# Kernel tuning notes

Measured on AMD Instinct MI355X. Metric: run time of the kernel, lower is better.

Reference implementation:

```python
import jax, jax.numpy as jnp
import numpy as np

N_NODES = 100000
N_EDGES = 1600000
NUM_FEATS = 128
HIDDEN = 16
NUM_CLASSES = 40


def setup_inputs() -> dict:
    key = jax.random.key(0)
    k1, k2, k3, k4, k5 = jax.random.split(key, 5)
    x = jax.random.normal(k1, (N_NODES, NUM_FEATS), dtype=jnp.float32)
    edge_weight = jax.random.uniform(k2, (N_EDGES,), dtype=jnp.float32)
    # Glorot-uniform linear weights (bias=False in the module)
    lim1 = float(np.sqrt(6.0 / (NUM_FEATS + HIDDEN)))
    lim2 = float(np.sqrt(6.0 / (HIDDEN + NUM_CLASSES)))
    W1 = jax.random.uniform(k3, (NUM_FEATS, HIDDEN), dtype=jnp.float32, minval=-lim1, maxval=lim1)
    W2 = jax.random.uniform(k4, (HIDDEN, NUM_CLASSES), dtype=jnp.float32, minval=-lim2, maxval=lim2)
    edge_index = jax.random.randint(k5, (2, N_EDGES), 0, N_NODES, dtype=jnp.int64)
    return {"x": x, "edge_weight": edge_weight, "W1": W1, "W2": W2, "edge_index": edge_index}


def _sgconv(h, W, src, dst, edge_weight, n):
    # SGConv (K=1): weighted neighbor aggregation + self loop (weight 1), then bias-free linear
    msg = edge_weight[:, None] * h[src]                      # [E, d] gather + scale
    agg = jax.ops.segment_sum(msg, dst, num_segments=n) + h  # scatter-add + self loop
    return agg @ W


def reference(x, edge_weight, W1, W2, edge_index):
    src, dst = edge_index[0], edge_index[1]
    n = x.shape[0]
    h = _sgconv(x, W1, src, dst, edge_weight, n)   # [N, 16]
    # dropout(p=0.5) is identity in eval mode
    h = _sgconv(h, W2, src, dst, edge_weight, n)   # [N, num_classes]
    return jax.nn.log_softmax(h, axis=1)
```

## Files before the change

kernel.cpp:

```cpp
#include <hip/hip_runtime.h>

#define NFEAT 128
#define HID 16
#define NCLS 40
#define BSHIFT 7
#define BNODES 128
#define CAP 2560
#define NBUCK_MAX 800
#define BIN_CHUNK 4096

#define SCALE1 262144.0f
#define SCALE2 65536.0f

__device__ __forceinline__ unsigned bf16_rne(float f) {
    unsigned u = __float_as_uint(f);
    return (u + 0x7FFFu + ((u >> 16) & 1u)) >> 16;
}
__device__ __forceinline__ float bf_lo(unsigned u) { return __uint_as_float(u << 16); }
__device__ __forceinline__ float bf_hi(unsigned u) { return __uint_as_float(u & 0xFFFF0000u); }


__global__ __launch_bounds__(256) void init_cursor_kernel(int* __restrict__ cursor, int nbuck)
{
    int i = blockIdx.x * 256 + threadIdx.x;
    if (i < nbuck) cursor[i] = i * CAP;
}

__global__ __launch_bounds__(256) void bin_kernel(const int* __restrict__ src,
                                                  const int* __restrict__ dst,
                                                  const float* __restrict__ ew,
                                                  int* __restrict__ cursor,
                                                  int2* __restrict__ slab,
                                                  int E, int nbuck)
{
    __shared__ int hist[NBUCK_MAX];
    __shared__ int runbase[NBUCK_MAX];
    int tid = threadIdx.x;
    for (int i = tid; i < NBUCK_MAX; i += 256) hist[i] = 0;
    __syncthreads();

    int base = blockIdx.x * BIN_CHUNK;
    int myd[16], mys[16], myw[16];
    #pragma unroll
    for (int k = 0; k < 16; ++k) {
        int e = base + k * 256 + tid;
        if (e < E) {
            myd[k] = dst[e];
            mys[k] = src[e];
            myw[k] = __float_as_int(ew[e]);
            atomicAdd(&hist[myd[k] >> BSHIFT], 1);
        } else myd[k] = -1;
    }
    __syncthreads();
    for (int i = tid; i < nbuck; i += 256) {
        int c = hist[i];
        runbase[i] = c ? atomicAdd(&cursor[i], c) : 0;
        hist[i] = 0;
    }
    __syncthreads();
    #pragma unroll
    for (int k = 0; k < 16; ++k) {
        int d = myd[k];
        if (d >= 0) {
            int b = d >> BSHIFT;
            int pos = runbase[b] + atomicAdd(&hist[b], 1);
            if (pos < (b + 1) * CAP)
                slab[pos] = make_int2(mys[k] | ((d & (BNODES - 1)) << 20), myw[k]);
        }
    }
}


__global__ __launch_bounds__(256) void gemm1_kernel(const float* __restrict__ x,
                                                    const float* __restrict__ W1,
                                                    unsigned short* __restrict__ h1b, int n)
{
    __shared__ float xs[64 * 132];
    __shared__ float ws[16 * 132];
    int tid = threadIdx.x;
    int r0 = blockIdx.x * 64;
    int rows = n - r0; if (rows > 64) rows = 64;

    const float4* xg = (const float4*)(x + (size_t)r0 * NFEAT);
    #pragma unroll
    for (int i = 0; i < 8; ++i) {
        int flat4 = i * 256 + tid;
        int row = flat4 >> 5, k4 = flat4 & 31;
        float4 v = make_float4(0.f, 0.f, 0.f, 0.f);
        if (row < rows) v = xg[flat4];
        *(float4*)&xs[row * 132 + k4 * 4] = v;
    }
    for (int i = tid; i < HID * NFEAT; i += 256) {
        int c = i >> 7, k = i & 127;
        ws[c * 132 + k] = W1[k * HID + c];
    }
    __syncthreads();

    int row = tid >> 2;
    int c0  = (tid & 3) * 4;
    float acc[4] = {0.f, 0.f, 0.f, 0.f};
    #pragma unroll 4
    for (int k4 = 0; k4 < 32; ++k4) {
        float4 xv = *(const float4*)&xs[row * 132 + k4 * 4];
        #pragma unroll
        for (int i = 0; i < 4; ++i) {
            float4 wv = *(const float4*)&ws[(c0 + i) * 132 + k4 * 4];
            acc[i] += xv.x * wv.x + xv.y * wv.y + xv.z * wv.z + xv.w * wv.w;
        }
    }
    if (row < rows) {
        unsigned lo = bf16_rne(acc[0]) | (bf16_rne(acc[1]) << 16);
        unsigned hi = bf16_rne(acc[2]) | (bf16_rne(acc[3]) << 16);
        *(uint2*)(h1b + (size_t)(r0 + row) * HID + c0) = make_uint2(lo, hi);
    }
}

__global__ __launch_bounds__(512) void gather_int_kernel(const uint4* __restrict__ hq,
                                                         const int* __restrict__ cursor,
                                                         const int2* __restrict__ slab,
                                                         float scale,
                                                         float4* __restrict__ outf,
                                                         uint4* __restrict__ outb,
                                                         int n)
{
    __shared__ int accum[HID * BNODES];
    int tid = threadIdx.x;
    #pragma unroll
    for (int i = tid; i < HID * BNODES; i += 512) accum[i] = 0;
    __syncthreads();

    int b = blockIdx.x;
    int beg = b * CAP;
    int cnt = cursor[b] - beg;
    if (cnt > CAP) cnt = CAP;

    int tasks = cnt * 2;
    for (int i = tid; i < tasks; i += 512) {
        int2 e = slab[beg + (i >> 1)];
        int p = i & 1;
        int s  = e.x & 0xFFFFF;
        int dl = (e.x >> 20) & (BNODES - 1);
        float wsc = __int_as_float(e.y) * scale;
        uint4 q = hq[(size_t)s * 2 + p];
        int* a = &accum[(p * 8) * BNODES + dl];
        atomicAdd(a + 0 * BNODES, __float2int_rn(wsc * bf_lo(q.x)));
        atomicAdd(a + 1 * BNODES, __float2int_rn(wsc * bf_hi(q.x)));
        atomicAdd(a + 2 * BNODES, __float2int_rn(wsc * bf_lo(q.y)));
        atomicAdd(a + 3 * BNODES, __float2int_rn(wsc * bf_hi(q.y)));
        atomicAdd(a + 4 * BNODES, __float2int_rn(wsc * bf_lo(q.z)));
        atomicAdd(a + 5 * BNODES, __float2int_rn(wsc * bf_hi(q.z)));
        atomicAdd(a + 6 * BNODES, __float2int_rn(wsc * bf_lo(q.w)));
        atomicAdd(a + 7 * BNODES, __float2int_rn(wsc * bf_hi(q.w)));
    }
    __syncthreads();

    float inv = 1.0f / scale;
    if (tid < BNODES * 2) {
        int dl = tid >> 1, p = tid & 1;
        int node = (b << BSHIFT) + dl;
        if (node < n) {
            uint4 qs = hq[(size_t)node * 2 + p];
            const int* a = &accum[(p * 8) * BNODES + dl];
            float r[8];
            r[0] = (float)a[0 * BNODES] * inv + bf_lo(qs.x);
            r[1] = (float)a[1 * BNODES] * inv + bf_hi(qs.x);
            r[2] = (float)a[2 * BNODES] * inv + bf_lo(qs.y);
            r[3] = (float)a[3 * BNODES] * inv + bf_hi(qs.y);
            r[4] = (float)a[4 * BNODES] * inv + bf_lo(qs.z);
            r[5] = (float)a[5 * BNODES] * inv + bf_hi(qs.z);
            r[6] = (float)a[6 * BNODES] * inv + bf_lo(qs.w);
            r[7] = (float)a[7 * BNODES] * inv + bf_hi(qs.w);
            if (outf) {
                outf[(size_t)node * 4 + p * 2 + 0] = make_float4(r[0], r[1], r[2], r[3]);
                outf[(size_t)node * 4 + p * 2 + 1] = make_float4(r[4], r[5], r[6], r[7]);
            }
            if (outb) {
                uint4 o;
                o.x = bf16_rne(r[0]) | (bf16_rne(r[1]) << 16);
                o.y = bf16_rne(r[2]) | (bf16_rne(r[3]) << 16);
                o.z = bf16_rne(r[4]) | (bf16_rne(r[5]) << 16);
                o.w = bf16_rne(r[6]) | (bf16_rne(r[7]) << 16);
                outb[(size_t)node * 2 + p] = o;
            }
        }
    }
}

__global__ __launch_bounds__(256) void gemm2_lsm_kernel(const float* __restrict__ h,
                                                        const float* __restrict__ W2,
                                                        float* __restrict__ out, int n)
{
    __shared__ float ws[HID * NCLS];
    int tid = threadIdx.x;
    for (int i = tid; i < HID * NCLS; i += 256) ws[i] = W2[i];
    __syncthreads();
    int r = blockIdx.x * 256 + tid;
    if (r >= n) return;

    float hr[HID];
    const float4* h4 = (const float4*)(h + (size_t)r * HID);
    #pragma unroll
    for (int i = 0; i < 4; ++i) {
        float4 v = h4[i];
        hr[i * 4 + 0] = v.x; hr[i * 4 + 1] = v.y; hr[i * 4 + 2] = v.z; hr[i * 4 + 3] = v.w;
    }
    float acc[NCLS];
    #pragma unroll
    for (int j = 0; j < NCLS; ++j) acc[j] = 0.f;
    #pragma unroll
    for (int k = 0; k < HID; ++k) {
        float hk = hr[k];
        #pragma unroll
        for (int j4 = 0; j4 < NCLS / 4; ++j4) {
            float4 w = *(const float4*)&ws[k * NCLS + j4 * 4];
            acc[j4 * 4 + 0] += hk * w.x;
            acc[j4 * 4 + 1] += hk * w.y;
            acc[j4 * 4 + 2] += hk * w.z;
            acc[j4 * 4 + 3] += hk * w.w;
        }
    }
    float m = acc[0];
    #pragma unroll
    for (int j = 1; j < NCLS; ++j) m = fmaxf(m, acc[j]);
    float ssum = 0.f;
    #pragma unroll
    for (int j = 0; j < NCLS; ++j) ssum += __expf(acc[j] - m);
    float l = m + __logf(ssum);
    float4* o4 = (float4*)(out + (size_t)r * NCLS);
    #pragma unroll
    for (int j4 = 0; j4 < NCLS / 4; ++j4)
        o4[j4] = make_float4(acc[j4 * 4 + 0] - l, acc[j4 * 4 + 1] - l,
                             acc[j4 * 4 + 2] - l, acc[j4 * 4 + 3] - l);
}

extern "C" void kernel_launch(void* const* d_in, const int* in_sizes, int n_in,
                              void* d_out, int out_size, void* d_ws, size_t ws_size,
                              hipStream_t stream)
{
    const float* x  = (const float*)d_in[0];
    const float* ew = (const float*)d_in[1];
    const float* W1 = (const float*)d_in[2];
    const float* W2 = (const float*)d_in[3];
    const int*   ei = (const int*)d_in[4];

    int n = in_sizes[0] / NFEAT;
    int E = in_sizes[1];
    const int* src = ei;
    const int* dst = ei + E;
    float* out = (float*)d_out;

    int nbuck = (n + BNODES - 1) >> BSHIFT;
    int nbin  = (E + BIN_CHUNK - 1) / BIN_CHUNK;

    char* w = (char*)d_ws;
    int*  cursor = (int*)w;  w += NBUCK_MAX * 4;
    w = (char*)(((size_t)w + 15) & ~(size_t)15);
    int2* slab   = (int2*)w; w += (size_t)NBUCK_MAX * CAP * 8;
    unsigned short* h1b = (unsigned short*)w; w += (size_t)n * HID * 2;
    unsigned short* h2b = (unsigned short*)w; w += (size_t)n * HID * 2;
    float* g2           = (float*)w;          w += (size_t)n * HID * 4;

    init_cursor_kernel<<<(nbuck + 255) / 256, 256, 0, stream>>>(cursor, nbuck);
    bin_kernel<<<nbin, 256, 0, stream>>>(src, dst, ew, cursor, slab, E, nbuck);

    gemm1_kernel<<<(n + 63) / 64, 256, 0, stream>>>(x, W1, h1b, n);
    gather_int_kernel<<<nbuck, 512, 0, stream>>>((const uint4*)h1b, cursor, slab,
                                                 SCALE1, nullptr, (uint4*)h2b, n);
    gather_int_kernel<<<nbuck, 512, 0, stream>>>((const uint4*)h2b, cursor, slab,
                                                 SCALE2, (float4*)g2, nullptr, n);
    gemm2_lsm_kernel<<<(n + 255) / 256, 256, 0, stream>>>(g2, W2, out, n);
}
```

Before: 185.2 us.

## Fuse binning with GEMM1 and second gather with GEMM2 plus log-softmax

Merges the edge-binning kernel and the first dense projection into one launch, where blocks are split by block index so both run concurrently. The second gather is fused with the W2 projection and log-softmax, so the fp32 intermediate no longer makes a round trip through global memory. The init-cursor kernel becomes a memset, with cursors now holding relative counts. This cuts launch count and intermediate traffic, at the cost of higher shared-memory and register use in the fused gather, where only 128 of 512 threads do the per-node epilogue.

```diff
diff --git a/kernel.cpp b/kernel.cpp
--- a/kernel.cpp
+++ b/kernel.cpp
@@ -20,108 +20,96 @@
 __device__ __forceinline__ float bf_hi(unsigned u) { return __uint_as_float(u & 0xFFFF0000u); }
 
 
-__global__ __launch_bounds__(256) void init_cursor_kernel(int* __restrict__ cursor, int nbuck)
-{
-    int i = blockIdx.x * 256 + threadIdx.x;
-    if (i < nbuck) cursor[i] = i * CAP;
-}
-
-__global__ __launch_bounds__(256) void bin_kernel(const int* __restrict__ src,
-                                                  const int* __restrict__ dst,
-                                                  const float* __restrict__ ew,
-                                                  int* __restrict__ cursor,
-                                                  int2* __restrict__ slab,
-                                                  int E, int nbuck)
-{
-    __shared__ int hist[NBUCK_MAX];
-    __shared__ int runbase[NBUCK_MAX];
+__global__ __launch_bounds__(256) void fused_bin_gemm1_kernel(
+        const int* __restrict__ src, const int* __restrict__ dst,
+        const float* __restrict__ ew, int* __restrict__ cursor,
+        int2* __restrict__ slab, int E, int nbuck, int nbin,
+        const float* __restrict__ x, const float* __restrict__ W1,
+        unsigned short* __restrict__ h1b, int n)
+{
+    __shared__ float smem[80 * 132];
     int tid = threadIdx.x;
-    for (int i = tid; i < NBUCK_MAX; i += 256) hist[i] = 0;
-    __syncthreads();
-
-    int base = blockIdx.x * BIN_CHUNK;
-    int myd[16], mys[16], myw[16];
-    #pragma unroll
-    for (int k = 0; k < 16; ++k) {
-        int e = base + k * 256 + tid;
-        if (e < E) {
-            myd[k] = dst[e];
-            mys[k] = src[e];
-            myw[k] = __float_as_int(ew[e]);
-            atomicAdd(&hist[myd[k] >> BSHIFT], 1);
-        } else myd[k] = -1;
-    }
-    __syncthreads();
-    for (int i = tid; i < nbuck; i += 256) {
-        int c = hist[i];
-        runbase[i] = c ? atomicAdd(&cursor[i], c) : 0;
-        hist[i] = 0;
-    }
-    __syncthreads();
-    #pragma unroll
-    for (int k = 0; k < 16; ++k) {
-        int d = myd[k];
-        if (d >= 0) {
-            int b = d >> BSHIFT;
-            int pos = runbase[b] + atomicAdd(&hist[b], 1);
-            if (pos < (b + 1) * CAP)
-                slab[pos] = make_int2(mys[k] | ((d & (BNODES - 1)) << 20), myw[k]);
-        }
-    }
-}
-
-
-__global__ __launch_bounds__(256) void gemm1_kernel(const float* __restrict__ x,
-                                                    const float* __restrict__ W1,
-                                                    unsigned short* __restrict__ h1b, int n)
-{
-    __shared__ float xs[64 * 132];
-    __shared__ float ws[16 * 132];
-    int tid = threadIdx.x;
-    int r0 = blockIdx.x * 64;
-    int rows = n - r0; if (rows > 64) rows = 64;
-
-    const float4* xg = (const float4*)(x + (size_t)r0 * NFEAT);
-    #pragma unroll
-    for (int i = 0; i < 8; ++i) {
-        int flat4 = i * 256 + tid;
-        int row = flat4 >> 5, k4 = flat4 & 31;
-        float4 v = make_float4(0.f, 0.f, 0.f, 0.f);
-        if (row < rows) v = xg[flat4];
-        *(float4*)&xs[row * 132 + k4 * 4] = v;
-    }
-    for (int i = tid; i < HID * NFEAT; i += 256) {
-        int c = i >> 7, k = i & 127;
-        ws[c * 132 + k] = W1[k * HID + c];
-    }
-    __syncthreads();
-
-    int row = tid >> 2;
-    int c0  = (tid & 3) * 4;
-    float acc[4] = {0.f, 0.f, 0.f, 0.f};
-    #pragma unroll 4
-    for (int k4 = 0; k4 < 32; ++k4) {
-        float4 xv = *(const float4*)&xs[row * 132 + k4 * 4];
+
+    if (blockIdx.x < (unsigned)nbin) {
+        int* hist    = (int*)smem;
+        int* runbase = hist + NBUCK_MAX;
+        for (int i = tid; i < NBUCK_MAX; i += 256) hist[i] = 0;
+        __syncthreads();
+
+        int base = blockIdx.x * BIN_CHUNK;
+        int myd[16], mys[16], myw[16];
         #pragma unroll
-        for (int i = 0; i < 4; ++i) {
-            float4 wv = *(const float4*)&ws[(c0 + i) * 132 + k4 * 4];
-            acc[i] += xv.x * wv.x + xv.y * wv.y + xv.z * wv.z + xv.w * wv.w;
-        }
-    }
-    if (row < rows) {
-        unsigned lo = bf16_rne(acc[0]) | (bf16_rne(acc[1]) << 16);
-        unsigned hi = bf16_rne(acc[2]) | (bf16_rne(acc[3]) << 16);
-        *(uint2*)(h1b + (size_t)(r0 + row) * HID + c0) = make_uint2(lo, hi);
-    }
-}
-
-__global__ __launch_bounds__(512) void gather_int_kernel(const uint4* __restrict__ hq,
-                                                         const int* __restrict__ cursor,
-                                                         const int2* __restrict__ slab,
-                                                         float scale,
-                                                         float4* __restrict__ outf,
-                                                         uint4* __restrict__ outb,
-                                                         int n)
+        for (int k = 0; k < 16; ++k) {
+            int e = base + k * 256 + tid;
+            if (e < E) {
+                myd[k] = dst[e];
+                mys[k] = src[e];
+                myw[k] = __float_as_int(ew[e]);
+                atomicAdd(&hist[myd[k] >> BSHIFT], 1);
+            } else myd[k] = -1;
+        }
+        __syncthreads();
+        for (int i = tid; i < nbuck; i += 256) {
+            int c = hist[i];
+            runbase[i] = c ? (i * CAP + atomicAdd(&cursor[i], c)) : 0;
+            hist[i] = 0;
+        }
+        __syncthreads();
+        #pragma unroll
+        for (int k = 0; k < 16; ++k) {
+            int d = myd[k];
+            if (d >= 0) {
+                int b = d >> BSHIFT;
+                int pos = runbase[b] + atomicAdd(&hist[b], 1);
+                if (pos < (b + 1) * CAP)
+                    slab[pos] = make_int2(mys[k] | ((d & (BNODES - 1)) << 20), myw[k]);
+            }
+        }
+    } else {
+        float* xs = smem;
+        float* ws = smem + 64 * 132;
+        int r0 = (blockIdx.x - nbin) * 64;
+        int rows = n - r0; if (rows > 64) rows = 64;
+
+        const float4* xg = (const float4*)(x + (size_t)r0 * NFEAT);
+        #pragma unroll
+        for (int i = 0; i < 8; ++i) {
+            int flat4 = i * 256 + tid;
+            int row = flat4 >> 5, k4 = flat4 & 31;
+            float4 v = make_float4(0.f, 0.f, 0.f, 0.f);
+            if (row < rows) v = xg[flat4];
+            *(float4*)&xs[row * 132 + k4 * 4] = v;
+        }
+        for (int i = tid; i < HID * NFEAT; i += 256) {
+            int c = i >> 7, k = i & 127;
+            ws[c * 132 + k] = W1[k * HID + c];
+        }
+        __syncthreads();
+
+        int row = tid >> 2;
+        int c0  = (tid & 3) * 4;
+        float acc[4] = {0.f, 0.f, 0.f, 0.f};
+        #pragma unroll 4
+        for (int k4 = 0; k4 < 32; ++k4) {
+            float4 xv = *(const float4*)&xs[row * 132 + k4 * 4];
+            #pragma unroll
+            for (int i = 0; i < 4; ++i) {
+                float4 wv = *(const float4*)&ws[(c0 + i) * 132 + k4 * 4];
+                acc[i] += xv.x * wv.x + xv.y * wv.y + xv.z * wv.z + xv.w * wv.w;
+            }
+        }
+        if (row < rows) {
+            unsigned lo = bf16_rne(acc[0]) | (bf16_rne(acc[1]) << 16);
+            unsigned hi = bf16_rne(acc[2]) | (bf16_rne(acc[3]) << 16);
+            *(uint2*)(h1b + (size_t)(r0 + row) * HID + c0) = make_uint2(lo, hi);
+        }
+    }
+}
+
+__global__ __launch_bounds__(512) void gather1_kernel(const uint4* __restrict__ hq,
+                                                      const int* __restrict__ cursor,
+                                                      const int2* __restrict__ slab,
+                                                      uint4* __restrict__ outb, int n)
 {
     __shared__ int accum[HID * BNODES];
     int tid = threadIdx.x;
@@ -131,8 +119,7 @@
 
     int b = blockIdx.x;
     int beg = b * CAP;
-    int cnt = cursor[b] - beg;
-    if (cnt > CAP) cnt = CAP;
+    int cnt = cursor[b]; if (cnt > CAP) cnt = CAP;
 
     int tasks = cnt * 2;
     for (int i = tid; i < tasks; i += 512) {
@@ -140,7 +127,7 @@
         int p = i & 1;
         int s  = e.x & 0xFFFFF;
         int dl = (e.x >> 20) & (BNODES - 1);
-        float wsc = __int_as_float(e.y) * scale;
+        float wsc = __int_as_float(e.y) * SCALE1;
         uint4 q = hq[(size_t)s * 2 + p];
         int* a = &accum[(p * 8) * BNODES + dl];
         atomicAdd(a + 0 * BNODES, __float2int_rn(wsc * bf_lo(q.x)));
@@ -154,83 +141,121 @@
     }
     __syncthreads();
 
-    float inv = 1.0f / scale;
+    const float inv = 1.0f / SCALE1;
     if (tid < BNODES * 2) {
         int dl = tid >> 1, p = tid & 1;
         int node = (b << BSHIFT) + dl;
         if (node < n) {
             uint4 qs = hq[(size_t)node * 2 + p];
             const int* a = &accum[(p * 8) * BNODES + dl];
-            float r[8];
-            r[0] = (float)a[0 * BNODES] * inv + bf_lo(qs.x);
-            r[1] = (float)a[1 * BNODES] * inv + bf_hi(qs.x);
-            r[2] = (float)a[2 * BNODES] * inv + bf_lo(qs.y);
-            r[3] = (float)a[3 * BNODES] * inv + bf_hi(qs.y);
-            r[4] = (float)a[4 * BNODES] * inv + bf_lo(qs.z);
-            r[5] = (float)a[5 * BNODES] * inv + bf_hi(qs.z);
-            r[6] = (float)a[6 * BNODES] * inv + bf_lo(qs.w);
-            r[7] = (float)a[7 * BNODES] * inv + bf_hi(qs.w);
-            if (outf) {
-                outf[(size_t)node * 4 + p * 2 + 0] = make_float4(r[0], r[1], r[2], r[3]);
-                outf[(size_t)node * 4 + p * 2 + 1] = make_float4(r[4], r[5], r[6], r[7]);
+            uint4 o;
+            o.x = bf16_rne((float)a[0 * BNODES] * inv + bf_lo(qs.x)) |
+                  (bf16_rne((float)a[1 * BNODES] * inv + bf_hi(qs.x)) << 16);
+            o.y = bf16_rne((float)a[2 * BNODES] * inv + bf_lo(qs.y)) |
+                  (bf16_rne((float)a[3 * BNODES] * inv + bf_hi(qs.y)) << 16);
+            o.z = bf16_rne((float)a[4 * BNODES] * inv + bf_lo(qs.z)) |
+                  (bf16_rne((float)a[5 * BNODES] * inv + bf_hi(qs.z)) << 16);
+            o.w = bf16_rne((float)a[6 * BNODES] * inv + bf_lo(qs.w)) |
+                  (bf16_rne((float)a[7 * BNODES] * inv + bf_hi(qs.w)) << 16);
+            outb[(size_t)node * 2 + p] = o;
+        }
+    }
+}
+
+#define ZPAD 41
+__global__ __launch_bounds__(512) void gather2_lsm_kernel(const uint4* __restrict__ hq,
+                                                          const int* __restrict__ cursor,
+                                                          const int2* __restrict__ slab,
+                                                          const float* __restrict__ W2,
+                                                          float* __restrict__ out, int n)
+{
+    __shared__ int   accum[HID * BNODES];
+    __shared__ float w2s[HID * NCLS];
+    __shared__ float zbuf[BNODES * ZPAD];
+    int tid = threadIdx.x;
+    #pragma unroll
+    for (int i = tid; i < HID * BNODES; i += 512) accum[i] = 0;
+    for (int i = tid; i < HID * NCLS; i += 512) w2s[i] = W2[i];
+    __syncthreads();
+
+    int b = blockIdx.x;
+    int beg = b * CAP;
+    int cnt = cursor[b]; if (cnt > CAP) cnt = CAP;
+    int node0 = b << BSHIFT;
+
+    int tasks = cnt * 2;
+    for (int i = tid; i < tasks; i += 512) {
+        int2 e = slab[beg + (i >> 1)];
+        int p = i & 1;
+        int s  = e.x & 0xFFFFF;
+        int dl = (e.x >> 20) & (BNODES - 1);
+        float wsc = __int_as_float(e.y) * SCALE2;
+        uint4 q = hq[(size_t)s * 2 + p];
+        int* a = &accum[(p * 8) * BNODES + dl];
+        atomicAdd(a + 0 * BNODES, __float2int_rn(wsc * bf_lo(q.x)));
+        atomicAdd(a + 1 * BNODES, __float2int_rn(wsc * bf_hi(q.x)));
+        atomicAdd(a + 2 * BNODES, __float2int_rn(wsc * bf_lo(q.y)));
+        atomicAdd(a + 3 * BNODES, __float2int_rn(wsc * bf_hi(q.y)));
+        atomicAdd(a + 4 * BNODES, __float2int_rn(wsc * bf_lo(q.z)));
+        atomicAdd(a + 5 * BNODES, __float2int_rn(wsc * bf_hi(q.z)));
+        atomicAdd(a + 6 * BNODES, __float2int_rn(wsc * bf_lo(q.w)));
+        atomicAdd(a + 7 * BNODES, __float2int_rn(wsc * bf_hi(q.w)));
+    }
+    __syncthreads();
+
+    const float inv = 1.0f / SCALE2;
+    if (tid < BNODES) {
+        int dl = tid;
+        int node = node0 + dl;
+        if (node < n) {
+            uint4 q0 = hq[(size_t)node * 2 + 0];
+            uint4 q1 = hq[(size_t)node * 2 + 1];
+            float r[HID];
+            r[0]  = (float)accum[ 0 * BNODES + dl] * inv + bf_lo(q0.x);
+            r[1]  = (float)accum[ 1 * BNODES + dl] * inv + bf_hi(q0.x);
+            r[2]  = (float)accum[ 2 * BNODES + dl] * inv + bf_lo(q0.y);
+            r[3]  = (float)accum[ 3 * BNODES + dl] * inv + bf_hi(q0.y);
+            r[4]  = (float)accum[ 4 * BNODES + dl] * inv + bf_lo(q0.z);
+            r[5]  = (float)accum[ 5 * BNODES + dl] * inv + bf_hi(q0.z);
+            r[6]  = (float)accum[ 6 * BNODES + dl] * inv + bf_lo(q0.w);
+            r[7]  = (float)accum[ 7 * BNODES + dl] * inv + bf_hi(q0.w);
+            r[8]  = (float)accum[ 8 * BNODES + dl] * inv + bf_lo(q1.x);
+            r[9]  = (float)accum[ 9 * BNODES + dl] * inv + bf_hi(q1.x);
+            r[10] = (float)accum[10 * BNODES + dl] * inv + bf_lo(q1.y);
+            r[11] = (float)accum[11 * BNODES + dl] * inv + bf_hi(q1.y);
+            r[12] = (float)accum[12 * BNODES + dl] * inv + bf_lo(q1.z);
+            r[13] = (float)accum[13 * BNODES + dl] * inv + bf_hi(q1.z);
+            r[14] = (float)accum[14 * BNODES + dl] * inv + bf_lo(q1.w);
+            r[15] = (float)accum[15 * BNODES + dl] * inv + bf_hi(q1.w);
+
+            float z[NCLS];
+            #pragma unroll
+            for (int j = 0; j < NCLS; ++j) z[j] = 0.f;
+            #pragma unroll
+            for (int f = 0; f < HID; ++f) {
+                float rf = r[f];
+                #pragma unroll
+                for (int j = 0; j < NCLS; ++j)
+                    z[j] += rf * w2s[f * NCLS + j];
             }
-            if (outb) {
-                uint4 o;
-                o.x = bf16_rne(r[0]) | (bf16_rne(r[1]) << 16);
-                o.y = bf16_rne(r[2]) | (bf16_rne(r[3]) << 16);
-                o.z = bf16_rne(r[4]) | (bf16_rne(r[5]) << 16);
-                o.w = bf16_rne(r[6]) | (bf16_rne(r[7]) << 16);
-                outb[(size_t)node * 2 + p] = o;
-            }
-        }
-    }
-}
-
-__global__ __launch_bounds__(256) void gemm2_lsm_kernel(const float* __restrict__ h,
-                                                        const float* __restrict__ W2,
-                                                        float* __restrict__ out, int n)
-{
-    __shared__ float ws[HID * NCLS];
-    int tid = threadIdx.x;
-    for (int i = tid; i < HID * NCLS; i += 256) ws[i] = W2[i];
-    __syncthreads();
-    int r = blockIdx.x * 256 + tid;
-    if (r >= n) return;
-
-    float hr[HID];
-    const float4* h4 = (const float4*)(h + (size_t)r * HID);
-    #pragma unroll
-    for (int i = 0; i < 4; ++i) {
-        float4 v = h4[i];
-        hr[i * 4 + 0] = v.x; hr[i * 4 + 1] = v.y; hr[i * 4 + 2] = v.z; hr[i * 4 + 3] = v.w;
-    }
-    float acc[NCLS];
-    #pragma unroll
-    for (int j = 0; j < NCLS; ++j) acc[j] = 0.f;
-    #pragma unroll
-    for (int k = 0; k < HID; ++k) {
-        float hk = hr[k];
-        #pragma unroll
-        for (int j4 = 0; j4 < NCLS / 4; ++j4) {
-            float4 w = *(const float4*)&ws[k * NCLS + j4 * 4];
-            acc[j4 * 4 + 0] += hk * w.x;
-            acc[j4 * 4 + 1] += hk * w.y;
-            acc[j4 * 4 + 2] += hk * w.z;
-            acc[j4 * 4 + 3] += hk * w.w;
-        }
-    }
-    float m = acc[0];
-    #pragma unroll
-    for (int j = 1; j < NCLS; ++j) m = fmaxf(m, acc[j]);
-    float ssum = 0.f;
-    #pragma unroll
-    for (int j = 0; j < NCLS; ++j) ssum += __expf(acc[j] - m);
-    float l = m + __logf(ssum);
-    float4* o4 = (float4*)(out + (size_t)r * NCLS);
-    #pragma unroll
-    for (int j4 = 0; j4 < NCLS / 4; ++j4)
-        o4[j4] = make_float4(acc[j4 * 4 + 0] - l, acc[j4 * 4 + 1] - l,
-                             acc[j4 * 4 + 2] - l, acc[j4 * 4 + 3] - l);
+            float m = z[0];
+            #pragma unroll
+            for (int j = 1; j < NCLS; ++j) m = fmaxf(m, z[j]);
+            float ssum = 0.f;
+            #pragma unroll
+            for (int j = 0; j < NCLS; ++j) ssum += __expf(z[j] - m);
+            float l = m + __logf(ssum);
+            #pragma unroll
+            for (int j = 0; j < NCLS; ++j) zbuf[dl * ZPAD + j] = z[j] - l;
+        }
+    }
+    __syncthreads();
+
+    for (int i = tid; i < BNODES * NCLS; i += 512) {
+        int nl = i / NCLS, j = i - nl * NCLS;
+        if (node0 + nl < n)
+            out[(size_t)node0 * NCLS + i] = zbuf[nl * ZPAD + j];
+    }
 }
 
 extern "C" void kernel_launch(void* const* d_in, const int* in_sizes, int n_in,
@@ -251,6 +276,7 @@
 
     int nbuck = (n + BNODES - 1) >> BSHIFT;
     int nbin  = (E + BIN_CHUNK - 1) / BIN_CHUNK;
+    int ngemm = (n + 63) / 64;
 
     char* w = (char*)d_ws;
     int*  cursor = (int*)w;  w += NBUCK_MAX * 4;
@@ -258,15 +284,12 @@
     int2* slab   = (int2*)w; w += (size_t)NBUCK_MAX * CAP * 8;
     unsigned short* h1b = (unsigned short*)w; w += (size_t)n * HID * 2;
     unsigned short* h2b = (unsigned short*)w; w += (size_t)n * HID * 2;
-    float* g2           = (float*)w;          w += (size_t)n * HID * 4;
-
-    init_cursor_kernel<<<(nbuck + 255) / 256, 256, 0, stream>>>(cursor, nbuck);
-    bin_kernel<<<nbin, 256, 0, stream>>>(src, dst, ew, cursor, slab, E, nbuck);
-
-    gemm1_kernel<<<(n + 63) / 64, 256, 0, stream>>>(x, W1, h1b, n);
-    gather_int_kernel<<<nbuck, 512, 0, stream>>>((const uint4*)h1b, cursor, slab,
-                                                 SCALE1, nullptr, (uint4*)h2b, n);
-    gather_int_kernel<<<nbuck, 512, 0, stream>>>((const uint4*)h2b, cursor, slab,
-                                                 SCALE2, (float4*)g2, nullptr, n);
-    gemm2_lsm_kernel<<<(n + 255) / 256, 256, 0, stream>>>(g2, W2, out, n);
-}
+
+    hipMemsetAsync(cursor, 0, (size_t)nbuck * 4, stream);
+    fused_bin_gemm1_kernel<<<nbin + ngemm, 256, 0, stream>>>(
+        src, dst, ew, cursor, slab, E, nbuck, nbin, x, W1, h1b, n);
+    gather1_kernel<<<nbuck, 512, 0, stream>>>((const uint4*)h1b, cursor, slab,
+                                              (uint4*)h2b, n);
+    gather2_lsm_kernel<<<nbuck, 512, 0, stream>>>((const uint4*)h2b, cursor, slab,
+                                                  W2, out, n);
+}
```

Result: no change. 186.0 us (+0.4%).
